# Performance work log

Measured on AMD Instinct MI355X. Metric: run time of the kernel, lower is better.

Reference implementation:

```python
import jax, jax.numpy as jnp
import numpy as np

B, S, D, H = 8, 1024, 1024, 16
DH = D // H


def setup_inputs() -> dict:
    key = jax.random.key(0)
    ks = jax.random.split(key, 7)
    scale = 1.0 / np.sqrt(DH)
    return {
        "sequences": jax.random.normal(ks[0], (B, S, D), dtype=jnp.float32),
        "Wq": jax.random.uniform(ks[1], (H, DH, DH), jnp.float32, -scale, scale),
        "bq": jax.random.uniform(ks[2], (H, DH), jnp.float32, -scale, scale),
        "Wk": jax.random.uniform(ks[3], (H, DH, DH), jnp.float32, -scale, scale),
        "bk": jax.random.uniform(ks[4], (H, DH), jnp.float32, -scale, scale),
        "Wv": jax.random.uniform(ks[5], (H, DH, DH), jnp.float32, -scale, scale),
        "bv": jax.random.uniform(ks[6], (H, DH), jnp.float32, -scale, scale),
    }


def reference(sequences, Wq, bq, Wk, bk, Wv, bv):
    # split channels into heads: [B,S,H,DH]
    x = sequences.reshape(B, S, H, DH)
    # per-head linear maps (torch Linear: y = x @ W.T + b)
    q = jnp.einsum("bshd,hed->bshe", x, Wq) + bq  # [B,S,H,DH]
    k = jnp.einsum("bshd,hed->bshe", x, Wk) + bk
    v = jnp.einsum("bshd,hed->bshe", x, Wv) + bv
    scores = jnp.einsum("bshd,bthd->bhst", q, k) / jnp.sqrt(jnp.asarray(DH, x.dtype))
    attn = jax.nn.softmax(scores, axis=-1)  # [B,H,S,S]
    out = jnp.einsum("bhst,bthd->bshd", attn, v)  # [B,S,H,DH]
    return out.reshape(B, S, D)
```

## Files before the change

### kernel.cpp

```cpp
#include <hip/hip_runtime.h>
#include <hip/hip_bf16.h>


constexpr int NB = 8, NS = 1024, ND = 1024, NH = 16, NDH = 64;

typedef __bf16 bf16x8 __attribute__((ext_vector_type(8)));
typedef float f32x4 __attribute__((ext_vector_type(4)));

__device__ __forceinline__ f32x4 mfma16(bf16x8 a, bf16x8 b, f32x4 c) {
  return __builtin_amdgcn_mfma_f32_16x16x32_bf16(a, b, c, 0, 0, 0);
}

__device__ __forceinline__ bf16x8 cvt2bf8(float4 lo, float4 hi) {
  bf16x8 r;
  r[0] = (__bf16)lo.x; r[1] = (__bf16)lo.y; r[2] = (__bf16)lo.z; r[3] = (__bf16)lo.w;
  r[4] = (__bf16)hi.x; r[5] = (__bf16)hi.y; r[6] = (__bf16)hi.z; r[7] = (__bf16)hi.w;
  return r;
}

__device__ __forceinline__ void gload16(const __hip_bfloat16* g, __hip_bfloat16* l) {
  __builtin_amdgcn_global_load_lds(
      (const __attribute__((address_space(1))) void*)g,
      (__attribute__((address_space(3))) void*)l, 16, 0, 0);
}

__device__ __forceinline__ unsigned pack_bf16(float hi, float lo) {
  unsigned uh = __builtin_bit_cast(unsigned, hi) + 0x8000u;
  unsigned ul = __builtin_bit_cast(unsigned, lo) + 0x8000u;
  return __builtin_amdgcn_perm(uh, ul, 0x07060302u);
}

__global__ __launch_bounds__(256) void qkv_proj_kernel(
    const float* __restrict__ x,
    const float* __restrict__ Wq, const float* __restrict__ bq,
    const float* __restrict__ Wk, const float* __restrict__ bk,
    const float* __restrict__ Wv, const float* __restrict__ bv,
    __hip_bfloat16* __restrict__ Qo, __hip_bfloat16* __restrict__ Ko,
    __hip_bfloat16* __restrict__ Vt) {
  __shared__ __align__(16) __hip_bfloat16 Wlds[3][NDH][72];
  const int tid = threadIdx.x;
  const int wave = tid >> 6, lane = tid & 63;
  const int m = lane & 15, quad = lane >> 4;
  const int h = blockIdx.x & (NH - 1);
  const int sblk = blockIdx.x >> 4;

  const float* Ws[3] = {Wq + h * 4096, Wk + h * 4096, Wv + h * 4096};
#pragma unroll
  for (int mt = 0; mt < 3; mt++) {
#pragma unroll
    for (int p = 0; p < 4; p++) {
      int idx = (p * 256 + tid) * 4;
      float4 v = *(const float4*)(Ws[mt] + idx);
      __align__(8) __hip_bfloat16 t4[4] = {
          __float2bfloat16(v.x), __float2bfloat16(v.y),
          __float2bfloat16(v.z), __float2bfloat16(v.w)};
      *(uint2*)&Wlds[mt][idx >> 6][idx & 63] = *(const uint2*)t4;
    }
  }
  __syncthreads();

  float bq4[4][4], bk4[4][4], bvv[4];
#pragma unroll
  for (int nt = 0; nt < 4; nt++) {
    float4 a = *(const float4*)(bq + h * 64 + nt * 16 + quad * 4);
    float4 c = *(const float4*)(bk + h * 64 + nt * 16 + quad * 4);
    bq4[nt][0] = a.x; bq4[nt][1] = a.y; bq4[nt][2] = a.z; bq4[nt][3] = a.w;
    bk4[nt][0] = c.x; bk4[nt][1] = c.y; bk4[nt][2] = c.z; bk4[nt][3] = c.w;
    bvv[nt] = bv[h * 64 + nt * 16 + m];
  }

  const int rowbase = sblk * 256 + wave * 64;
  bf16x8 Xf[4][2];
#pragma unroll
  for (int st = 0; st < 4; st++) {
    const float* xp = x + (size_t)(rowbase + st * 16 + m) * ND + h * NDH + quad * 8;
#pragma unroll
    for (int c = 0; c < 2; c++) {
      float4 lo = *(const float4*)(xp + c * 32);
      float4 hi = *(const float4*)(xp + c * 32 + 4);
      Xf[st][c] = cvt2bf8(lo, hi);
    }
  }

  const int b = rowbase >> 10;
  const int s0 = rowbase & 1023;
  const float qscale = 0.18033688011112042f;

#pragma unroll
  for (int mt = 0; mt < 3; mt++) {
#pragma unroll
    for (int nt = 0; nt < 4; nt++) {
      bf16x8 w0 = *(const bf16x8*)&Wlds[mt][nt * 16 + m][quad * 8];
      bf16x8 w1 = *(const bf16x8*)&Wlds[mt][nt * 16 + m][32 + quad * 8];
#pragma unroll
      for (int st = 0; st < 4; st++) {
        f32x4 acc = {0.f, 0.f, 0.f, 0.f};
        if (mt < 2) {
          acc = mfma16(w0, Xf[st][0], acc);
          acc = mfma16(w1, Xf[st][1], acc);
          const int srow = s0 + st * 16 + m;
          __align__(8) __hip_bfloat16 t4[4];
          if (mt == 0) {
#pragma unroll
            for (int r = 0; r < 4; r++)
              t4[r] = __float2bfloat16((acc[r] + bq4[nt][r]) * qscale);
            *(uint2*)(Qo + ((size_t)(b * NH + h) * NS + srow) * NDH +
                      nt * 16 + quad * 4) = *(const uint2*)t4;
          } else {
#pragma unroll
            for (int r = 0; r < 4; r++)
              t4[r] = __float2bfloat16(acc[r] + bk4[nt][r]);
            *(uint2*)(Ko + ((size_t)(b * NH + h) * NS + srow) * NDH +
                      nt * 16 + quad * 4) = *(const uint2*)t4;
          }
        } else {
          acc = mfma16(Xf[st][0], w0, acc);
          acc = mfma16(Xf[st][1], w1, acc);
          __align__(8) __hip_bfloat16 t4[4];
#pragma unroll
          for (int r = 0; r < 4; r++) t4[r] = __float2bfloat16(acc[r] + bvv[nt]);
          *(uint2*)(Vt + ((size_t)(b * NH + h) * NDH + nt * 16 + m) * NS + s0 +
                    st * 16 + quad * 4) = *(const uint2*)t4;
        }
      }
    }
  }
}

__global__ __launch_bounds__(256, 4) void attn_kernel(
    const __hip_bfloat16* __restrict__ Q,
    const __hip_bfloat16* __restrict__ K,
    const __hip_bfloat16* __restrict__ Vt,
    float* __restrict__ out) {
  __shared__ __align__(16) __hip_bfloat16 Kt[2][64][64];
  __shared__ __align__(16) __hip_bfloat16 Vl[2][64][64];
  __shared__ __align__(16) __hip_bfloat16 Pt[4][16][64];

  const int tid = threadIdx.x;
  const int wave = tid >> 6, lane = tid & 63;
  const int m = lane & 15, quad = lane >> 4;

  const int xcd = blockIdx.x & 7;
  const int j = blockIdx.x >> 3;
  const int bh = xcd * 16 + (j & 15);
  const int qblk = j >> 4;
  const int qbase = qblk * 128 + wave * 32;

  const __hip_bfloat16* Qp = Q + (size_t)bh * NS * NDH;
  const __hip_bfloat16* Kp = K + (size_t)bh * NS * NDH;
  const __hip_bfloat16* Vp = Vt + (size_t)bh * NDH * NS;

  bf16x8 Bq[2][2];
#pragma unroll
  for (int g = 0; g < 2; g++)
#pragma unroll
    for (int c = 0; c < 2; c++)
      Bq[g][c] = *(const bf16x8*)(Qp + (size_t)(qbase + g * 16 + m) * NDH +
                                  c * 32 + quad * 8);

  f32x4 accO[2][4];
  f32x4 lsum[2];
#pragma unroll
  for (int g = 0; g < 2; g++) {
    lsum[g] = (f32x4){0.f, 0.f, 0.f, 0.f};
#pragma unroll
    for (int nt = 0; nt < 4; nt++) accO[g][nt] = (f32x4){0.f, 0.f, 0.f, 0.f};
  }
  bf16x8 ones;
#pragma unroll
  for (int i = 0; i < 8; i++) ones[i] = (__bf16)1.0f;

  const int r8 = lane >> 3;
  const int cs = (lane & 7) ^ r8;
  const int pc = quad ^ (m & 7);

#define STAGE(buf, tb)                                                        \
  {                                                                           \
    _Pragma("unroll") for (int p = 0; p < 2; p++) {                           \
      const int row = wave * 16 + p * 8;                                      \
      gload16(Kp + (size_t)((tb) * 64 + row + r8) * NDH + cs * 8,             \
              &Kt[buf][row][0]);                                              \
      gload16(Vp + (size_t)(row + r8) * NS + (tb) * 64 + cs * 8,              \
              &Vl[buf][row][0]);                                              \
    }                                                                         \
  }

  STAGE(0, 0);

  for (int tb = 0; tb < NS / 64; tb++) {
    const int cur = tb & 1;
    __syncthreads();
    if (tb + 1 < NS / 64) STAGE(cur ^ 1, tb + 1);

#pragma unroll
    for (int g = 0; g < 2; g++) {
      f32x4 sc[4];
#pragma unroll
      for (int nt = 0; nt < 4; nt++) {
        bf16x8 k0 = *(const bf16x8*)&Kt[cur][nt * 16 + m][pc * 8];
        bf16x8 k1 = *(const bf16x8*)&Kt[cur][nt * 16 + m][(pc ^ 4) * 8];
        f32x4 a = {0.f, 0.f, 0.f, 0.f};
        a = mfma16(k0, Bq[g][0], a);
        a = mfma16(k1, Bq[g][1], a);
        sc[nt] = a;
      }
#pragma unroll
      for (int nt = 0; nt < 4; nt++) {
        float e0 = __builtin_exp2f(sc[nt][0]);
        float e1 = __builtin_exp2f(sc[nt][1]);
        float e2 = __builtin_exp2f(sc[nt][2]);
        float e3 = __builtin_exp2f(sc[nt][3]);
        uint2 w;
        w.x = pack_bf16(e1, e0);
        w.y = pack_bf16(e3, e2);
        const int c8 = (nt * 2 + (quad >> 1)) ^ (m & 7);
        *(uint2*)&Pt[wave][m][c8 * 8 + (quad & 1) * 4] = w;
      }
      __builtin_amdgcn_fence(__ATOMIC_SEQ_CST, "wavefront");
      bf16x8 P0 = *(const bf16x8*)&Pt[wave][m][pc * 8];
      bf16x8 P1 = *(const bf16x8*)&Pt[wave][m][(pc ^ 4) * 8];
      lsum[g] = mfma16(P0, ones, lsum[g]);
      lsum[g] = mfma16(P1, ones, lsum[g]);
#pragma unroll
      for (int nt = 0; nt < 4; nt++) {
        bf16x8 v0 = *(const bf16x8*)&Vl[cur][nt * 16 + m][pc * 8];
        bf16x8 v1 = *(const bf16x8*)&Vl[cur][nt * 16 + m][(pc ^ 4) * 8];
        accO[g][nt] = mfma16(P0, v0, accO[g][nt]);
        accO[g][nt] = mfma16(P1, v1, accO[g][nt]);
      }
    }
  }
#undef STAGE

  const int b = bh >> 4, h = bh & (NH - 1);
#pragma unroll
  for (int g = 0; g < 2; g++) {
#pragma unroll
    for (int r = 0; r < 4; r++) {
      float inv = 1.0f / lsum[g][r];
      int srow = qbase + g * 16 + quad * 4 + r;
      float* op = out + (size_t)(b * NS + srow) * ND + h * NDH;
#pragma unroll
      for (int nt = 0; nt < 4; nt++) op[nt * 16 + m] = accO[g][nt][r] * inv;
    }
  }
}

extern "C" void kernel_launch(void* const* d_in, const int* in_sizes, int n_in,
                              void* d_out, int out_size, void* d_ws, size_t ws_size,
                              hipStream_t stream) {
  const float* x  = (const float*)d_in[0];
  const float* Wq = (const float*)d_in[1];
  const float* bq = (const float*)d_in[2];
  const float* Wk = (const float*)d_in[3];
  const float* bk = (const float*)d_in[4];
  const float* Wv = (const float*)d_in[5];
  const float* bv = (const float*)d_in[6];
  float* out = (float*)d_out;

  const size_t elems = (size_t)NB * NH * NS * NDH;
  __hip_bfloat16* Qw = (__hip_bfloat16*)d_ws;
  __hip_bfloat16* Kw = Qw + elems;
  __hip_bfloat16* Vw = Kw + elems;

  qkv_proj_kernel<<<512, 256, 0, stream>>>(x, Wq, bq, Wk, bk, Wv, bv, Qw, Kw, Vw);
  attn_kernel<<<1024, 256, 0, stream>>>(Qw, Kw, Vw, out);
}
```

Before: 161.1 us.

## Keep P in registers via 16x16x16 MFMA and double queries per wave

The exponentiated score tile is no longer written to and reread from LDS. It is packed straight into registers and fed to 16x16x16 bf16 MFMAs, whose input layout matches the score accumulator layout. Each wave now handles 64 queries instead of 32, and K and V fragments are loaded once per tile and reused across four query groups, so the grid is halved and launch bounds relaxed to 2 blocks per CU. The cost is higher register pressure and lower occupancy. The fast hardware exp2 intrinsic is also used.

Measured after the change: 149.6 us. -7.1%, faster.

```diff
diff --git a/kernel.cpp b/kernel.cpp
--- a/kernel.cpp
+++ b/kernel.cpp
@@ -5,10 +5,30 @@
 constexpr int NB = 8, NS = 1024, ND = 1024, NH = 16, NDH = 64;
 
 typedef __bf16 bf16x8 __attribute__((ext_vector_type(8)));
+typedef short bf16x4s __attribute__((ext_vector_type(4)));
 typedef float f32x4 __attribute__((ext_vector_type(4)));
 
 __device__ __forceinline__ f32x4 mfma16(bf16x8 a, bf16x8 b, f32x4 c) {
   return __builtin_amdgcn_mfma_f32_16x16x32_bf16(a, b, c, 0, 0, 0);
+}
+
+__device__ __forceinline__ f32x4 mfma16k16(bf16x4s a, bf16x4s b, f32x4 c) {
+#if __has_builtin(__builtin_amdgcn_mfma_f32_16x16x16bf16_1k)
+  return __builtin_amdgcn_mfma_f32_16x16x16bf16_1k(a, b, c, 0, 0, 0);
+#else
+  f32x4 d;
+  asm("v_mfma_f32_16x16x16_bf16 %0, %1, %2, %3"
+      : "=v"(d) : "v"(a), "v"(b), "v"(c));
+  return d;
+#endif
+}
+
+__device__ __forceinline__ float fast_exp2(float x) {
+#if __has_builtin(__builtin_amdgcn_exp2f)
+  return __builtin_amdgcn_exp2f(x);
+#else
+  return __builtin_exp2f(x);
+#endif
 }
 
 __device__ __forceinline__ bf16x8 cvt2bf8(float4 lo, float4 hi) {
@@ -127,14 +147,13 @@
   }
 }
 
-__global__ __launch_bounds__(256, 4) void attn_kernel(
+__global__ __launch_bounds__(256, 2) void attn_kernel(
     const __hip_bfloat16* __restrict__ Q,
     const __hip_bfloat16* __restrict__ K,
     const __hip_bfloat16* __restrict__ Vt,
     float* __restrict__ out) {
   __shared__ __align__(16) __hip_bfloat16 Kt[2][64][64];
   __shared__ __align__(16) __hip_bfloat16 Vl[2][64][64];
-  __shared__ __align__(16) __hip_bfloat16 Pt[4][16][64];
 
   const int tid = threadIdx.x;
   const int wave = tid >> 6, lane = tid & 63;
@@ -144,35 +163,37 @@
   const int j = blockIdx.x >> 3;
   const int bh = xcd * 16 + (j & 15);
   const int qblk = j >> 4;
-  const int qbase = qblk * 128 + wave * 32;
+  const int qbase = qblk * 256 + wave * 64;
 
   const __hip_bfloat16* Qp = Q + (size_t)bh * NS * NDH;
   const __hip_bfloat16* Kp = K + (size_t)bh * NS * NDH;
   const __hip_bfloat16* Vp = Vt + (size_t)bh * NDH * NS;
 
-  bf16x8 Bq[2][2];
-#pragma unroll
-  for (int g = 0; g < 2; g++)
+  bf16x8 Bq[4][2];
+#pragma unroll
+  for (int g = 0; g < 4; g++)
 #pragma unroll
     for (int c = 0; c < 2; c++)
       Bq[g][c] = *(const bf16x8*)(Qp + (size_t)(qbase + g * 16 + m) * NDH +
                                   c * 32 + quad * 8);
 
-  f32x4 accO[2][4];
-  f32x4 lsum[2];
-#pragma unroll
-  for (int g = 0; g < 2; g++) {
+  f32x4 accO[4][4];
+  f32x4 lsum[4];
+#pragma unroll
+  for (int g = 0; g < 4; g++) {
     lsum[g] = (f32x4){0.f, 0.f, 0.f, 0.f};
 #pragma unroll
     for (int nt = 0; nt < 4; nt++) accO[g][nt] = (f32x4){0.f, 0.f, 0.f, 0.f};
   }
-  bf16x8 ones;
-#pragma unroll
-  for (int i = 0; i < 8; i++) ones[i] = (__bf16)1.0f;
+  const bf16x4s ones4 = {0x3F80, 0x3F80, 0x3F80, 0x3F80};
 
   const int r8 = lane >> 3;
   const int cs = (lane & 7) ^ r8;
   const int pc = quad ^ (m & 7);
+  int voffs[4];
+#pragma unroll
+  for (int s = 0; s < 4; s++)
+    voffs[s] = (((2 * s) | (quad >> 1)) ^ (m & 7)) * 8 + (quad & 1) * 4;
 
 #define STAGE(buf, tb)                                                        \
   {                                                                           \
@@ -192,49 +213,56 @@
     __syncthreads();
     if (tb + 1 < NS / 64) STAGE(cur ^ 1, tb + 1);
 
-#pragma unroll
-    for (int g = 0; g < 2; g++) {
+    bf16x8 kf[4][2];
+#pragma unroll
+    for (int nt = 0; nt < 4; nt++) {
+      kf[nt][0] = *(const bf16x8*)&Kt[cur][nt * 16 + m][pc * 8];
+      kf[nt][1] = *(const bf16x8*)&Kt[cur][nt * 16 + m][(pc ^ 4) * 8];
+    }
+    bf16x4s vf[4][4];
+#pragma unroll
+    for (int nt = 0; nt < 4; nt++)
+#pragma unroll
+      for (int s = 0; s < 4; s++)
+        vf[nt][s] = __builtin_bit_cast(
+            bf16x4s, *(const uint2*)&Vl[cur][nt * 16 + m][voffs[s]]);
+
+#pragma unroll
+    for (int g = 0; g < 4; g++) {
       f32x4 sc[4];
 #pragma unroll
-      for (int nt = 0; nt < 4; nt++) {
-        bf16x8 k0 = *(const bf16x8*)&Kt[cur][nt * 16 + m][pc * 8];
-        bf16x8 k1 = *(const bf16x8*)&Kt[cur][nt * 16 + m][(pc ^ 4) * 8];
+      for (int s = 0; s < 4; s++) {
         f32x4 a = {0.f, 0.f, 0.f, 0.f};
-        a = mfma16(k0, Bq[g][0], a);
-        a = mfma16(k1, Bq[g][1], a);
-        sc[nt] = a;
+        a = mfma16(kf[s][0], Bq[g][0], a);
+        a = mfma16(kf[s][1], Bq[g][1], a);
+        sc[s] = a;
       }
-#pragma unroll
-      for (int nt = 0; nt < 4; nt++) {
-        float e0 = __builtin_exp2f(sc[nt][0]);
-        float e1 = __builtin_exp2f(sc[nt][1]);
-        float e2 = __builtin_exp2f(sc[nt][2]);
-        float e3 = __builtin_exp2f(sc[nt][3]);
+      bf16x4s Pa[4];
+#pragma unroll
+      for (int s = 0; s < 4; s++) {
+        float e0 = fast_exp2(sc[s][0]);
+        float e1 = fast_exp2(sc[s][1]);
+        float e2 = fast_exp2(sc[s][2]);
+        float e3 = fast_exp2(sc[s][3]);
         uint2 w;
         w.x = pack_bf16(e1, e0);
         w.y = pack_bf16(e3, e2);
-        const int c8 = (nt * 2 + (quad >> 1)) ^ (m & 7);
-        *(uint2*)&Pt[wave][m][c8 * 8 + (quad & 1) * 4] = w;
+        Pa[s] = __builtin_bit_cast(bf16x4s, w);
       }
-      __builtin_amdgcn_fence(__ATOMIC_SEQ_CST, "wavefront");
-      bf16x8 P0 = *(const bf16x8*)&Pt[wave][m][pc * 8];
-      bf16x8 P1 = *(const bf16x8*)&Pt[wave][m][(pc ^ 4) * 8];
-      lsum[g] = mfma16(P0, ones, lsum[g]);
-      lsum[g] = mfma16(P1, ones, lsum[g]);
-#pragma unroll
-      for (int nt = 0; nt < 4; nt++) {
-        bf16x8 v0 = *(const bf16x8*)&Vl[cur][nt * 16 + m][pc * 8];
-        bf16x8 v1 = *(const bf16x8*)&Vl[cur][nt * 16 + m][(pc ^ 4) * 8];
-        accO[g][nt] = mfma16(P0, v0, accO[g][nt]);
-        accO[g][nt] = mfma16(P1, v1, accO[g][nt]);
-      }
+#pragma unroll
+      for (int s = 0; s < 4; s++) lsum[g] = mfma16k16(Pa[s], ones4, lsum[g]);
+#pragma unroll
+      for (int nt = 0; nt < 4; nt++)
+#pragma unroll
+        for (int s = 0; s < 4; s++)
+          accO[g][nt] = mfma16k16(Pa[s], vf[nt][s], accO[g][nt]);
     }
   }
 #undef STAGE
 
   const int b = bh >> 4, h = bh & (NH - 1);
 #pragma unroll
-  for (int g = 0; g < 2; g++) {
+  for (int g = 0; g < 4; g++) {
 #pragma unroll
     for (int r = 0; r < 4; r++) {
       float inv = 1.0f / lsum[g][r];
@@ -264,5 +292,5 @@
   __hip_bfloat16* Vw = Kw + elems;
 
   qkv_proj_kernel<<<512, 256, 0, stream>>>(x, Wq, bq, Wk, bk, Wv, bv, Qw, Kw, Vw);
-  attn_kernel<<<1024, 256, 0, stream>>>(Qw, Kw, Vw, out);
-}
+  attn_kernel<<<512, 256, 0, stream>>>(Qw, Kw, Vw, out);
+}
```
